# Kernel tuning notes

Hardware: AMD Instinct MI355X
Metric: run time of the kernel (lower is better)

## Reference

```python
import jax, jax.numpy as jnp
import numpy as np

N = 50000      # nodes
E = 400000     # edges (avg degree 8)
C = 128        # dim_single (node_dim)
DP = 64        # dim_pair (edge_dim)
HID = 256      # dim_egnn_hidden
DEPTH = 4      # depth_equivariant
M_IN = 2 * C + DP  # node_mlp / coord_mlp input dim = 320


def setup_inputs() -> dict:
    key = jax.random.key(0)
    ks = jax.random.split(key, 12)
    def w(k, shape, fan):
        return jax.random.normal(k, shape, jnp.float32) / np.float32(np.sqrt(fan))
    return {
        'single': jax.random.normal(ks[0], (N, C), jnp.float32),
        'pair': jax.random.normal(ks[1], (1,), jnp.float32),  # unused (se3t/ipa disabled)
        'coords': jax.random.normal(ks[2], (N, 3), jnp.float32),
        'edge_index': jax.random.randint(ks[3], (2, E), 0, N, jnp.int32),
        'edge_dist': jax.random.uniform(ks[4], (E,), jnp.float32),
        # stacked per-layer EGNN params (leading DEPTH axis, consumed by lax.scan)
        'We1': w(ks[5], (DEPTH, 1, DP), 1), 'be1': jnp.zeros((DEPTH, DP), jnp.float32),
        'We2': w(ks[6], (DEPTH, DP, DP), DP), 'be2': jnp.zeros((DEPTH, DP), jnp.float32),
        'Wn1': w(ks[7], (DEPTH, M_IN, HID), M_IN), 'bn1': jnp.zeros((DEPTH, HID), jnp.float32),
        'Wn2': w(ks[8], (DEPTH, HID, C), HID), 'bn2': jnp.zeros((DEPTH, C), jnp.float32),
        'Wc1': w(ks[9], (DEPTH, M_IN, HID), M_IN), 'bc1': jnp.zeros((DEPTH, HID), jnp.float32),
        'Wc2': w(ks[10], (DEPTH, HID, 1), HID),  # coord_mlp final layer has no bias
        'gamma': jnp.ones((C,), jnp.float32), 'beta': jnp.zeros((C,), jnp.float32),
    }


def _egnn_stack(h, x, edge_index, edge_dist, params):
    src, dst = edge_index[0], edge_index[1]
    n_nodes = h.shape[0]
    def layer(carry, p):
        h, x = carry
        We1, be1, We2, be2, Wn1, bn1, Wn2, bn2, Wc1, bc1, Wc2 = p
        # edge_mlp(edge_dist)
        ea = jax.nn.silu(edge_dist[:, None] @ We1 + be1) @ We2 + be2        # [E, DP]
        # gather -> concat -> MLP (message)
        mi = jnp.concatenate([h[src], h[dst], ea], axis=-1)                 # [E, 2C+DP]
        m = jax.nn.silu(mi @ Wn1 + bn1) @ Wn2 + bn2                         # [E, C]
        h = h + jax.ops.segment_sum(m, dst, num_segments=n_nodes)          # index_add on dst
        # coordinate update
        cw = jax.nn.silu(mi @ Wc1 + bc1) @ Wc2                              # [E, 1]
        x = x + jax.ops.segment_sum(cw * (x[src] - x[dst]), dst, num_segments=n_nodes)
        return (h, x), None
    (h, x), _ = jax.lax.scan(layer, (h, x), params)
    return h, x


def reference(single, pair, coords, edge_index, edge_dist,
              We1, be1, We2, be2, Wn1, bn1, Wn2, bn2, Wc1, bc1, Wc2,
              gamma, beta):
    h, x = _egnn_stack(single, coords, edge_index, edge_dist,
                       (We1, be1, We2, be2, Wn1, bn1, Wn2, bn2, Wc1, bc1, Wc2))
    # final LayerNorm (eps=1e-5, matching nn.LayerNorm default)
    mu = h.mean(-1, keepdims=True)
    var = ((h - mu) ** 2).mean(-1, keepdims=True)
    out = gamma * (h - mu) * jax.lax.rsqrt(var + 1e-5) + beta
    return out, x
```

## Files before the change

kernel.cpp:

```cpp
#include <hip/hip_runtime.h>
#include <hip/hip_bf16.h>
#include <math.h>

#define NN 50000
#define NE 400000
#define CD 128
#define EPB 64
#define HBINS 50176

typedef __attribute__((ext_vector_type(8))) short bf16x8;
typedef __attribute__((ext_vector_type(4))) float f32x4;

__device__ __forceinline__ float silu_f(float z) {
    return z * __builtin_amdgcn_rcpf(1.f + __expf(-z));
}
__device__ __forceinline__ unsigned short f2bf(float x) {
    unsigned int u = __float_as_uint(x);
    u = (u + 0x7FFFu + ((u >> 16) & 1u)) >> 16;
    return (unsigned short)u;
}
__device__ __forceinline__ float bf2f(unsigned short h) {
    return __uint_as_float(((unsigned int)h) << 16);
}
__device__ __forceinline__ unsigned pk_bf16(float a, float b) {
    union { __hip_bfloat162 h2; unsigned u; } cv;
    cv.h2 = __float22bfloat162_rn(make_float2(a, b));
    return cv.u;
}

__global__ __launch_bounds__(256) void hist_kernel(
        const int* __restrict__ dst, int* __restrict__ hist)
{
    int e = blockIdx.x * 256 + threadIdx.x;
    if (e < NE) atomicAdd(&hist[dst[e]], 1);
}

__global__ __launch_bounds__(256) void scan1_kernel(
        const int* __restrict__ hist, int* __restrict__ offs, int* __restrict__ bsum)
{
    __shared__ int sh[256];
    const int t = threadIdx.x;
    const int i = blockIdx.x * 256 + t;
    int v = hist[i];
    sh[t] = v;
    __syncthreads();
    for (int off = 1; off < 256; off <<= 1) {
        int x = (t >= off) ? sh[t - off] : 0;
        __syncthreads();
        sh[t] += x;
        __syncthreads();
    }
    offs[i] = sh[t] - v;
    if (t == 255) bsum[blockIdx.x] = sh[t];
}

__global__ __launch_bounds__(256) void scan2_kernel(int* __restrict__ bsum)
{
    __shared__ int sh[256];
    const int t = threadIdx.x;
    int v = (t < 196) ? bsum[t] : 0;
    sh[t] = v;
    __syncthreads();
    for (int off = 1; off < 256; off <<= 1) {
        int x = (t >= off) ? sh[t - off] : 0;
        __syncthreads();
        sh[t] += x;
        __syncthreads();
    }
    if (t < 196) bsum[t] = sh[t] - v;
}

__global__ __launch_bounds__(256) void scan3_kernel(
        const int* __restrict__ offs, const int* __restrict__ bsum,
        int* __restrict__ cursor)
{
    const int i = blockIdx.x * 256 + threadIdx.x;
    cursor[i] = offs[i] + bsum[blockIdx.x];
}

__global__ __launch_bounds__(256) void scatter_kernel(
        const int* __restrict__ eidx, const float* __restrict__ edist,
        int* __restrict__ cursor,
        int* __restrict__ ssrc, int* __restrict__ sdst, float* __restrict__ sdist)
{
    int e = blockIdx.x * 256 + threadIdx.x;
    if (e < NE) {
        int d = eidx[NE + e];
        int p = atomicAdd(&cursor[d], 1);
        ssrc[p] = eidx[e];
        sdst[p] = d;
        sdist[p] = edist[e];
    }
}

__global__ __launch_bounds__(64) void wbig_prep(
        const float* __restrict__ We2, const float* __restrict__ Wn1,
        const float* __restrict__ Wc1, unsigned short* __restrict__ wbig)
{
    const int l = blockIdx.y;
    const int ntile = blockIdx.x / 10;
    const int ks = blockIdx.x % 10;
    const int lane = threadIdx.x;
    const int n = ntile * 16 + (lane & 15);
    const int kbase = ks * 32 + (lane >> 4) * 8;
    const float* Wn1l = Wn1 + (size_t)l * 320 * 256;
    const float* Wc1l = Wc1 + (size_t)l * 320 * 256;
    const float* We2l = We2 + (size_t)l * 64 * 64;
    const float* W1 = (n < 256) ? Wn1l : Wc1l;
    const int nn = n & 255;
    unsigned short* outp = wbig + ((((size_t)l * 32 + ntile) * 10 + ks) * 64 + lane) * 8;
    #pragma unroll
    for (int j = 0; j < 8; ++j) {
        int k = kbase + j;
        float val;
        if (k < 256) {
            val = W1[(size_t)k * 256 + nn];
        } else {
            int i = k - 256;
            float acc = 0.f;
            #pragma unroll 8
            for (int jj = 0; jj < 64; ++jj)
                acc += We2l[i * 64 + jj] * W1[(size_t)(256 + jj) * 256 + nn];
            val = acc;
        }
        outp[j] = f2bf(val);
    }
}

__global__ __launch_bounds__(64) void wn2_prep(
        const float* __restrict__ Wn2, unsigned short* __restrict__ wn2s)
{
    const int l = blockIdx.y;
    const int ntile = blockIdx.x / 8;
    const int ks = blockIdx.x % 8;
    const int lane = threadIdx.x;
    const int n = ntile * 16 + (lane & 15);
    const int kbase = ks * 32 + (lane >> 4) * 8;
    const float* Wn2l = Wn2 + (size_t)l * 256 * 128;
    unsigned short* outp = wn2s + ((((size_t)l * 8 + ntile) * 8 + ks) * 64 + lane) * 8;
    #pragma unroll
    for (int j = 0; j < 8; ++j)
        outp[j] = f2bf(Wn2l[(size_t)(kbase + j) * 128 + n]);
}

__global__ __launch_bounds__(512) void cep_prep(
        const float* __restrict__ be2,
        const float* __restrict__ Wn1, const float* __restrict__ Wc1,
        const float* __restrict__ bn1, const float* __restrict__ bc1,
        float* __restrict__ cep)
{
    const int l = blockIdx.x;
    const int j = threadIdx.x;
    const int jj = j & 255;
    const float* W1 = ((j < 256) ? Wn1 : Wc1) + (size_t)l * 320 * 256;
    const float* be2l = be2 + l * 64;
    float acc = (j < 256) ? bn1[l * 256 + jj] : bc1[l * 256 + jj];
    #pragma unroll 8
    for (int k = 0; k < 64; ++k)
        acc += be2l[k] * W1[(size_t)(256 + k) * 256 + jj];
    cep[l * 512 + j] = acc;
}

__global__ __launch_bounds__(256) void conv_kernel(
        const float* __restrict__ h, unsigned short* __restrict__ hbf)
{
    const int i = (blockIdx.x * 256 + threadIdx.x) * 4;
    float4 v = *(const float4*)(h + i);
    *(uint2*)(hbf + i) = make_uint2(pk_bf16(v.x, v.y), pk_bf16(v.z, v.w));
}

__global__ __launch_bounds__(512, 4) void edge_kernel(
        const int* __restrict__ ssrc, const int* __restrict__ sdst,
        const float* __restrict__ sdist,
        const float* __restrict__ We1l, const float* __restrict__ be1l,
        const unsigned short* __restrict__ hbf,
        const unsigned short* __restrict__ wbig_l,
        const float* __restrict__ cep_l,
        const float* __restrict__ Wc2l,
        const float* __restrict__ x_in,
        float* __restrict__ Tbar, float* __restrict__ x_out)
{
    __shared__ __align__(16) unsigned short s_A[EPB][328];
    __shared__ __align__(16) unsigned short s_t[EPB][264];
    __shared__ __align__(16) float s_cw[EPB][4];
    __shared__ int s_src[EPB], s_dst[EPB];
    __shared__ unsigned long long s_mask;

    const int tid = threadIdx.x;
    const int eb = blockIdx.x * EPB;

    if (tid < EPB) {
        int dv = sdst[eb + tid];
        s_src[tid] = ssrc[eb + tid];
        s_dst[tid] = dv;
        int nxt = (tid == EPB - 1) ? -1 : sdst[eb + tid + 1];
        unsigned long long mk = __ballot(dv != nxt);
        if (tid == 0) s_mask = mk;
    }
    {
        const int e = tid >> 3;
        const int j0 = (tid & 7) * 8;
        const float d = sdist[eb + e];
        unsigned tmp[4];
        #pragma unroll
        for (int j = 0; j < 4; ++j) {
            float a = silu_f(d * We1l[j0 + 2 * j] + be1l[j0 + 2 * j]);
            float b = silu_f(d * We1l[j0 + 2 * j + 1] + be1l[j0 + 2 * j + 1]);
            tmp[j] = pk_bf16(a, b);
        }
        *(bf16x8*)&s_A[e][j0 + 256] = *(const bf16x8*)tmp;
    }
    __syncthreads();

    #pragma unroll
    for (int it = 0; it < 4; ++it) {
        const int c = tid + it * 512;
        const int row = c >> 5, ch = c & 31;
        const int node = (ch < 16) ? s_src[row] : s_dst[row];
        const int koff = (ch & 15) * 8;
        bf16x8 v = *(const bf16x8*)(hbf + (size_t)node * CD + koff);
        *(bf16x8*)&s_A[row][ch * 8] = v;
    }
    __syncthreads();

    const int wave = tid >> 6, lane = tid & 63;
    const int m = lane & 15, q = lane >> 4;

    f32x4 acc[4][4];
    #pragma unroll
    for (int nt = 0; nt < 4; ++nt)
        #pragma unroll
        for (int mt = 0; mt < 4; ++mt)
            acc[nt][mt] = (f32x4){0.f, 0.f, 0.f, 0.f};

    #pragma unroll
    for (int ks = 0; ks < 10; ++ks) {
        const int koff = ks * 32 + q * 8;
        bf16x8 ef[4];
        #pragma unroll
        for (int mt = 0; mt < 4; ++mt)
            ef[mt] = *(const bf16x8*)&s_A[mt * 16 + m][koff];
        #pragma unroll
        for (int nt = 0; nt < 4; ++nt) {
            bf16x8 wf = *(const bf16x8*)(wbig_l +
                ((size_t)((wave * 4 + nt) * 10 + ks) * 64 + lane) * 8);
            #pragma unroll
            for (int mt = 0; mt < 4; ++mt)
                acc[nt][mt] = __builtin_amdgcn_mfma_f32_16x16x32_bf16(wf, ef[mt], acc[nt][mt], 0, 0, 0);
        }
    }

    if (wave < 4) {
        #pragma unroll
        for (int nt = 0; nt < 4; ++nt) {
            const int c0 = (wave * 4 + nt) * 16 + q * 4;
            const float4 ce = *(const float4*)&cep_l[c0];
            #pragma unroll
            for (int mt = 0; mt < 4; ++mt) {
                float t0 = silu_f(acc[nt][mt][0] + ce.x);
                float t1 = silu_f(acc[nt][mt][1] + ce.y);
                float t2 = silu_f(acc[nt][mt][2] + ce.z);
                float t3 = silu_f(acc[nt][mt][3] + ce.w);
                *(uint2*)&s_t[mt * 16 + m][c0] =
                    make_uint2(pk_bf16(t0, t1), pk_bf16(t2, t3));
            }
        }
    } else {
        float p[4] = {0.f, 0.f, 0.f, 0.f};
        #pragma unroll
        for (int nt = 0; nt < 4; ++nt) {
            const int c0 = (wave * 4 + nt) * 16 + q * 4;
            const float4 ce = *(const float4*)&cep_l[c0];
            const float4 wv = *(const float4*)&Wc2l[c0 - 256];
            #pragma unroll
            for (int mt = 0; mt < 4; ++mt) {
                p[mt] += silu_f(acc[nt][mt][0] + ce.x) * wv.x;
                p[mt] += silu_f(acc[nt][mt][1] + ce.y) * wv.y;
                p[mt] += silu_f(acc[nt][mt][2] + ce.z) * wv.z;
                p[mt] += silu_f(acc[nt][mt][3] + ce.w) * wv.w;
            }
        }
        #pragma unroll
        for (int mt = 0; mt < 4; ++mt) {
            p[mt] += __shfl_xor(p[mt], 16);
            p[mt] += __shfl_xor(p[mt], 32);
        }
        if (lane < 16) {
            #pragma unroll
            for (int mt = 0; mt < 4; ++mt)
                s_cw[mt * 16 + lane][wave - 4] = p[mt];
        }
    }
    __syncthreads();

    if (wave < 2) {
        const unsigned long long mask = s_mask;
        const int colb = wave * 128 + lane * 2;
        float a0 = 0.f, a1 = 0.f;
        #pragma unroll 8
        for (int e = 0; e < EPB; ++e) {
            unsigned v = *(const unsigned*)&s_t[e][colb];
            a0 += bf2f((unsigned short)v);
            a1 += bf2f((unsigned short)(v >> 16));
            if ((mask >> e) & 1ull) {
                int dn = s_dst[e];
                atomicAdd(&Tbar[(size_t)dn * 256 + colb], a0);
                atomicAdd(&Tbar[(size_t)dn * 256 + colb + 1], a1);
                a0 = 0.f; a1 = 0.f;
            }
        }
    } else if (wave == 2) {
        const int e = lane;
        float4 pv = *(const float4*)&s_cw[e][0];
        float cw = pv.x + pv.y + pv.z + pv.w;
        int sn = s_src[e], dn = s_dst[e];
        float dx0 = x_in[sn * 3 + 0] - x_in[dn * 3 + 0];
        float dx1 = x_in[sn * 3 + 1] - x_in[dn * 3 + 1];
        float dx2 = x_in[sn * 3 + 2] - x_in[dn * 3 + 2];
        atomicAdd(&x_out[dn * 3 + 0], cw * dx0);
        atomicAdd(&x_out[dn * 3 + 1], cw * dx1);
        atomicAdd(&x_out[dn * 3 + 2], cw * dx2);
    }
}

__global__ __launch_bounds__(256) void node_kernel(
        const float* __restrict__ Tbar, const int* __restrict__ deg,
        const unsigned short* __restrict__ wn2_l, const float* __restrict__ bn2l,
        float* __restrict__ h, unsigned short* __restrict__ hbf)
{
    const int nb = blockIdx.x * 64;
    const int tid = threadIdx.x;
    const int wave = tid >> 6, lane = tid & 63;
    const int m = lane & 15, q = lane >> 4;

    f32x4 acc[2][4];
    #pragma unroll
    for (int nt = 0; nt < 2; ++nt)
        #pragma unroll
        for (int mt = 0; mt < 4; ++mt)
            acc[nt][mt] = (f32x4){0.f, 0.f, 0.f, 0.f};

    #pragma unroll
    for (int ks = 0; ks < 8; ++ks) {
        bf16x8 af[4];
        #pragma unroll
        for (int mt = 0; mt < 4; ++mt) {
            const int node = nb + mt * 16 + m;
            if (node < NN) {
                const float* tp = Tbar + (size_t)node * 256 + ks * 32 + q * 8;
                float4 f0 = *(const float4*)tp;
                float4 f1 = *(const float4*)(tp + 4);
                unsigned u[4] = { pk_bf16(f0.x, f0.y), pk_bf16(f0.z, f0.w),
                                  pk_bf16(f1.x, f1.y), pk_bf16(f1.z, f1.w) };
                af[mt] = *(const bf16x8*)u;
            } else {
                af[mt] = (bf16x8){0,0,0,0,0,0,0,0};
            }
        }
        #pragma unroll
        for (int nt = 0; nt < 2; ++nt) {
            bf16x8 wf = *(const bf16x8*)(wn2_l +
                ((size_t)((wave * 2 + nt) * 8 + ks) * 64 + lane) * 8);
            #pragma unroll
            for (int mt = 0; mt < 4; ++mt)
                acc[nt][mt] = __builtin_amdgcn_mfma_f32_16x16x32_bf16(af[mt], wf, acc[nt][mt], 0, 0, 0);
        }
    }
    #pragma unroll
    for (int nt = 0; nt < 2; ++nt) {
        const int col = (wave * 2 + nt) * 16 + m;
        const float bb = bn2l[col];
        #pragma unroll
        for (int mt = 0; mt < 4; ++mt) {
            #pragma unroll
            for (int i = 0; i < 4; ++i) {
                const int node = nb + mt * 16 + q * 4 + i;
                if (node < NN) {
                    float val = acc[nt][mt][i] + (float)deg[node] * bb
                              + h[(size_t)node * CD + col];
                    h[(size_t)node * CD + col] = val;
                    hbf[(size_t)node * CD + col] = f2bf(val);
                }
            }
        }
    }
}

__global__ __launch_bounds__(256) void final_kernel(
        const float* __restrict__ h, const float* __restrict__ x,
        const float* __restrict__ gamma, const float* __restrict__ beta,
        float* __restrict__ out)
{
    const int lane = threadIdx.x & 63;
    const int wave = threadIdx.x >> 6;
    const int n = blockIdx.x * 4 + wave;
    float v0 = h[(size_t)n * CD + lane];
    float v1 = h[(size_t)n * CD + 64 + lane];
    float ssum = v0 + v1;
    for (int off = 32; off; off >>= 1) ssum += __shfl_xor(ssum, off);
    float mu = ssum * (1.f / 128.f);
    float d0 = v0 - mu, d1 = v1 - mu;
    float sq = d0 * d0 + d1 * d1;
    for (int off = 32; off; off >>= 1) sq += __shfl_xor(sq, off);
    float rstd = rsqrtf(sq * (1.f / 128.f) + 1e-5f);
    out[(size_t)n * CD + lane]      = gamma[lane]      * d0 * rstd + beta[lane];
    out[(size_t)n * CD + 64 + lane] = gamma[64 + lane] * d1 * rstd + beta[64 + lane];
    if (threadIdx.x < 12) {
        int nn = blockIdx.x * 4 + threadIdx.x / 3;
        int c = threadIdx.x % 3;
        out[(size_t)NN * CD + nn * 3 + c] = x[nn * 3 + c];
    }
}

static inline size_t align_up(size_t v) { return (v + 255) & ~(size_t)255; }

extern "C" void kernel_launch(void* const* d_in, const int* in_sizes, int n_in,
                              void* d_out, int out_size, void* d_ws, size_t ws_size,
                              hipStream_t stream)
{
    const float* single = (const float*)d_in[0];
    const float* coords = (const float*)d_in[2];
    const int*   eidx   = (const int*)d_in[3];
    const float* edist  = (const float*)d_in[4];
    const float* We1 = (const float*)d_in[5];
    const float* be1 = (const float*)d_in[6];
    const float* We2 = (const float*)d_in[7];
    const float* be2 = (const float*)d_in[8];
    const float* Wn1 = (const float*)d_in[9];
    const float* bn1 = (const float*)d_in[10];
    const float* Wn2 = (const float*)d_in[11];
    const float* bn2 = (const float*)d_in[12];
    const float* Wc1 = (const float*)d_in[13];
    const float* bc1 = (const float*)d_in[14];
    const float* Wc2 = (const float*)d_in[15];
    const float* gamma = (const float*)d_in[16];
    const float* beta  = (const float*)d_in[17];
    float* out = (float*)d_out;

    char* w = (char*)d_ws;
    float* h0  = (float*)w;  w += align_up((size_t)NN * CD * 4);
    float* x0  = (float*)w;  w += align_up((size_t)NN * 3 * 4);
    float* x1  = (float*)w;  w += align_up((size_t)NN * 3 * 4);
    unsigned short* hbf  = (unsigned short*)w; w += align_up((size_t)NN * CD * 2);
    unsigned short* wbig = (unsigned short*)w; w += align_up((size_t)4 * 512 * 320 * 2);
    unsigned short* wn2s = (unsigned short*)w; w += align_up((size_t)4 * 256 * 128 * 2);
    float* cep = (float*)w;  w += align_up((size_t)4 * 512 * 4);
    int* hist   = (int*)w;   w += align_up((size_t)HBINS * 4);
    int* offs   = (int*)w;   w += align_up((size_t)HBINS * 4);
    int* cursor = (int*)w;   w += align_up((size_t)HBINS * 4);
    int* bsum   = (int*)w;   w += align_up((size_t)256 * 4);
    int* ssrc   = (int*)w;   w += align_up((size_t)NE * 4);
    int* sdst   = (int*)w;   w += align_up((size_t)NE * 4);
    float* sdist = (float*)w; w += align_up((size_t)NE * 4);
    float* Tbar = (float*)w; w += align_up((size_t)NN * 256 * 4);

    hipMemsetAsync(hist, 0, (size_t)HBINS * 4, stream);
    hist_kernel<<<(NE + 255) / 256, 256, 0, stream>>>(eidx + NE, hist);
    scan1_kernel<<<HBINS / 256, 256, 0, stream>>>(hist, offs, bsum);
    scan2_kernel<<<1, 256, 0, stream>>>(bsum);
    scan3_kernel<<<HBINS / 256, 256, 0, stream>>>(offs, bsum, cursor);
    scatter_kernel<<<(NE + 255) / 256, 256, 0, stream>>>(eidx, edist, cursor, ssrc, sdst, sdist);

    wbig_prep<<<dim3(320, 4), 64, 0, stream>>>(We2, Wn1, Wc1, wbig);
    wn2_prep<<<dim3(64, 4), 64, 0, stream>>>(Wn2, wn2s);
    cep_prep<<<4, 512, 0, stream>>>(be2, Wn1, Wc1, bn1, bc1, cep);

    hipMemcpyAsync(h0, single, (size_t)NN * CD * 4, hipMemcpyDeviceToDevice, stream);
    hipMemcpyAsync(x0, coords, (size_t)NN * 3 * 4, hipMemcpyDeviceToDevice, stream);
    conv_kernel<<<(NN * CD) / 1024, 256, 0, stream>>>(single, hbf);

    float* xc = x0; float* xn = x1;
    for (int l = 0; l < 4; ++l) {
        hipMemsetAsync(Tbar, 0, (size_t)NN * 256 * 4, stream);
        hipMemcpyAsync(xn, xc, (size_t)NN * 3 * 4, hipMemcpyDeviceToDevice, stream);
        edge_kernel<<<NE / EPB, 512, 0, stream>>>(
            ssrc, sdst, sdist,
            We1 + l * 64, be1 + l * 64,
            hbf,
            wbig + (size_t)l * 512 * 320,
            cep + l * 512,
            Wc2 + l * 256,
            xc, Tbar, xn);
        node_kernel<<<(NN + 63) / 64, 256, 0, stream>>>(
            Tbar, hist,
            wn2s + (size_t)l * 256 * 128,
            bn2 + l * CD, h0, hbf);
        float* t = xc; xc = xn; xn = t;
    }
    final_kernel<<<NN / 4, 256, 0, stream>>>(h0, xc, gamma, beta, out);
}
```

Baseline: 1.462 ms.

## Make edge kernel persistent with double-buffered async LDS gathers and MFMA segment reduction

The edge kernel becomes persistent: 512 blocks each loop over a contiguous range of 64-edge tiles. While the current tile is being computed, the next tile's node features are prefetched into double-buffered LDS with global_load_lds, using an XOR swizzle. The per-destination segment sum, previously a serial loop with atomics, is now an MFMA against a 0/1 run-indicator matrix, followed by one atomic per run. This trades occupancy (launch bounds drop to 2 blocks per SM) and adds extra syncs per tile in return for hiding gather latency.

```diff
diff --git a/kernel.cpp b/kernel.cpp
--- a/kernel.cpp
+++ b/kernel.cpp
@@ -5,7 +5,8 @@
 #define NN 50000
 #define NE 400000
 #define CD 128
-#define EPB 64
+#define NT 6250
+#define NB 512
 #define HBINS 50176
 
 typedef __attribute__((ext_vector_type(8))) short bf16x8;
@@ -26,6 +27,11 @@
     union { __hip_bfloat162 h2; unsigned u; } cv;
     cv.h2 = __float22bfloat162_rn(make_float2(a, b));
     return cv.u;
+}
+__device__ __forceinline__ void gload_lds16(const unsigned short* g, unsigned short* l) {
+    __builtin_amdgcn_global_load_lds(
+        (const __attribute__((address_space(1))) unsigned int*)g,
+        (__attribute__((address_space(3))) unsigned int*)l, 16, 0, 0);
 }
 
 __global__ __launch_bounds__(256) void hist_kernel(
@@ -169,7 +175,7 @@
     *(uint2*)(hbf + i) = make_uint2(pk_bf16(v.x, v.y), pk_bf16(v.z, v.w));
 }
 
-__global__ __launch_bounds__(512, 4) void edge_kernel(
+__global__ __launch_bounds__(512, 2) void edge_kernel(
         const int* __restrict__ ssrc, const int* __restrict__ sdst,
         const float* __restrict__ sdist,
         const float* __restrict__ We1l, const float* __restrict__ be1l,
@@ -180,27 +186,37 @@
         const float* __restrict__ x_in,
         float* __restrict__ Tbar, float* __restrict__ x_out)
 {
-    __shared__ __align__(16) unsigned short s_A[EPB][328];
-    __shared__ __align__(16) unsigned short s_t[EPB][264];
-    __shared__ __align__(16) float s_cw[EPB][4];
-    __shared__ int s_src[EPB], s_dst[EPB];
+    __shared__ __align__(16) unsigned short s_h[2][64 * 256];
+    __shared__ __align__(16) unsigned short s_e[2][64][72];
+    __shared__ __align__(16) unsigned short s_tT[256][72];
+    __shared__ __align__(16) unsigned short s_G[64][72];
+    __shared__ __align__(16) float s_cw[64][4];
+    __shared__ int s_sd[2][2][64];
+    __shared__ int s_rdst[64];
     __shared__ unsigned long long s_mask;
 
     const int tid = threadIdx.x;
-    const int eb = blockIdx.x * EPB;
-
-    if (tid < EPB) {
-        int dv = sdst[eb + tid];
-        s_src[tid] = ssrc[eb + tid];
-        s_dst[tid] = dv;
-        int nxt = (tid == EPB - 1) ? -1 : sdst[eb + tid + 1];
-        unsigned long long mk = __ballot(dv != nxt);
-        if (tid == 0) s_mask = mk;
-    }
-    {
-        const int e = tid >> 3;
-        const int j0 = (tid & 7) * 8;
-        const float d = sdist[eb + e];
+    const int wave = tid >> 6, lane = tid & 63;
+    const int m = lane & 15, q = lane >> 4;
+    const int lo = (int)(((long long)blockIdx.x * NT) / NB);
+    const int hi = (int)(((long long)(blockIdx.x + 1) * NT) / NB);
+
+    auto stage_issue = [&](int T) {
+        const int pp = T & 1;
+        #pragma unroll
+        for (int it = 0; it < 4; ++it) {
+            const int slot = it * 512 + wave * 64 + lane;
+            const int row = slot >> 5;
+            const int c = (slot & 31) ^ (row & 7);
+            const int node = s_sd[pp][c >> 4][row];
+            gload_lds16(hbf + (size_t)node * CD + (c & 15) * 8,
+                        &s_h[pp][slot * 8]);
+        }
+    };
+    auto ea_comp = [&](int T) {
+        const int pp = T & 1;
+        const int e = tid >> 3, j0 = (tid & 7) * 8;
+        const float d = sdist[T * 64 + e];
         unsigned tmp[4];
         #pragma unroll
         for (int j = 0; j < 4; ++j) {
@@ -208,118 +224,203 @@
             float b = silu_f(d * We1l[j0 + 2 * j + 1] + be1l[j0 + 2 * j + 1]);
             tmp[j] = pk_bf16(a, b);
         }
-        *(bf16x8*)&s_A[e][j0 + 256] = *(const bf16x8*)tmp;
+        *(bf16x8*)&s_e[pp][e][j0] = *(const bf16x8*)tmp;
+    };
+
+    int sv_c = 0, dv_c = 0, sv_n = 0, dv_n = 0;
+    float xs0 = 0.f, xs1 = 0.f, xs2 = 0.f, xd0 = 0.f, xd1 = 0.f, xd2 = 0.f;
+
+    if (wave == 0) {
+        sv_c = ssrc[lo * 64 + lane];
+        dv_c = sdst[lo * 64 + lane];
+        s_sd[lo & 1][0][lane] = sv_c;
+        s_sd[lo & 1][1][lane] = dv_c;
     }
     __syncthreads();
-
-    #pragma unroll
-    for (int it = 0; it < 4; ++it) {
-        const int c = tid + it * 512;
-        const int row = c >> 5, ch = c & 31;
-        const int node = (ch < 16) ? s_src[row] : s_dst[row];
-        const int koff = (ch & 15) * 8;
-        bf16x8 v = *(const bf16x8*)(hbf + (size_t)node * CD + koff);
-        *(bf16x8*)&s_A[row][ch * 8] = v;
-    }
-    __syncthreads();
-
-    const int wave = tid >> 6, lane = tid & 63;
-    const int m = lane & 15, q = lane >> 4;
-
-    f32x4 acc[4][4];
-    #pragma unroll
-    for (int nt = 0; nt < 4; ++nt)
-        #pragma unroll
-        for (int mt = 0; mt < 4; ++mt)
-            acc[nt][mt] = (f32x4){0.f, 0.f, 0.f, 0.f};
-
-    #pragma unroll
-    for (int ks = 0; ks < 10; ++ks) {
-        const int koff = ks * 32 + q * 8;
-        bf16x8 ef[4];
-        #pragma unroll
-        for (int mt = 0; mt < 4; ++mt)
-            ef[mt] = *(const bf16x8*)&s_A[mt * 16 + m][koff];
-        #pragma unroll
-        for (int nt = 0; nt < 4; ++nt) {
-            bf16x8 wf = *(const bf16x8*)(wbig_l +
-                ((size_t)((wave * 4 + nt) * 10 + ks) * 64 + lane) * 8);
+    stage_issue(lo);
+    ea_comp(lo);
+    if (wave == 0 && lo + 1 < hi) {
+        sv_n = ssrc[(lo + 1) * 64 + lane];
+        dv_n = sdst[(lo + 1) * 64 + lane];
+        s_sd[(lo + 1) & 1][0][lane] = sv_n;
+        s_sd[(lo + 1) & 1][1][lane] = dv_n;
+    }
+
+    for (int T = lo; T < hi; ++T) {
+        const int pb = T & 1;
+
+        for (int i = tid; i < 64 * 72 / 2; i += 512)
+            ((unsigned*)s_G)[i] = 0u;
+        __syncthreads();
+
+        if (wave == 0) {
+            int nxtd = __shfl(dv_c, lane + 1);
+            if (lane == 63) nxtd = -1;
+            unsigned long long mk = __ballot(dv_c != nxtd);
+            int rid = __popcll(mk & ((1ull << lane) - 1ull));
+            s_G[rid][lane ^ ((rid & 3) << 3)] = 0x3F80;
+            if ((mk >> lane) & 1ull) s_rdst[rid] = dv_c;
+            if (lane == 0) s_mask = mk;
+            xs0 = x_in[sv_c * 3];     xs1 = x_in[sv_c * 3 + 1]; xs2 = x_in[sv_c * 3 + 2];
+            xd0 = x_in[dv_c * 3];     xd1 = x_in[dv_c * 3 + 1]; xd2 = x_in[dv_c * 3 + 2];
+        }
+        if (T + 1 < hi) stage_issue(T + 1);
+
+        f32x4 acc[4][4];
+        #pragma unroll
+        for (int nt = 0; nt < 4; ++nt)
             #pragma unroll
             for (int mt = 0; mt < 4; ++mt)
-                acc[nt][mt] = __builtin_amdgcn_mfma_f32_16x16x32_bf16(wf, ef[mt], acc[nt][mt], 0, 0, 0);
-        }
-    }
-
-    if (wave < 4) {
-        #pragma unroll
-        for (int nt = 0; nt < 4; ++nt) {
-            const int c0 = (wave * 4 + nt) * 16 + q * 4;
-            const float4 ce = *(const float4*)&cep_l[c0];
+                acc[nt][mt] = (f32x4){0.f, 0.f, 0.f, 0.f};
+
+        if (wave < 4) {
+            #pragma unroll
+            for (int ks = 0; ks < 10; ++ks) {
+                bf16x8 ef[4];
+                #pragma unroll
+                for (int mt = 0; mt < 4; ++mt) {
+                    const int row = mt * 16 + m;
+                    ef[mt] = (ks < 8)
+                        ? *(const bf16x8*)&s_h[pb][row * 256 + ((ks * 4 + q) ^ (m & 7)) * 8]
+                        : *(const bf16x8*)&s_e[pb][row][(ks - 8) * 32 + q * 8];
+                }
+                #pragma unroll
+                for (int nt = 0; nt < 4; ++nt) {
+                    bf16x8 wf = *(const bf16x8*)(wbig_l +
+                        ((size_t)((wave * 4 + nt) * 10 + ks) * 64 + lane) * 8);
+                    #pragma unroll
+                    for (int mt = 0; mt < 4; ++mt)
+                        acc[nt][mt] = __builtin_amdgcn_mfma_f32_16x16x32_bf16(
+                            ef[mt], wf, acc[nt][mt], 0, 0, 0);
+                }
+            }
+        } else {
+            #pragma unroll
+            for (int ks = 0; ks < 10; ++ks) {
+                bf16x8 ef[4];
+                #pragma unroll
+                for (int mt = 0; mt < 4; ++mt) {
+                    const int row = mt * 16 + m;
+                    ef[mt] = (ks < 8)
+                        ? *(const bf16x8*)&s_h[pb][row * 256 + ((ks * 4 + q) ^ (m & 7)) * 8]
+                        : *(const bf16x8*)&s_e[pb][row][(ks - 8) * 32 + q * 8];
+                }
+                #pragma unroll
+                for (int nt = 0; nt < 4; ++nt) {
+                    bf16x8 wf = *(const bf16x8*)(wbig_l +
+                        ((size_t)((wave * 4 + nt) * 10 + ks) * 64 + lane) * 8);
+                    #pragma unroll
+                    for (int mt = 0; mt < 4; ++mt)
+                        acc[nt][mt] = __builtin_amdgcn_mfma_f32_16x16x32_bf16(
+                            wf, ef[mt], acc[nt][mt], 0, 0, 0);
+                }
+            }
+        }
+        __syncthreads();
+
+        if (wave < 4) {
+            #pragma unroll
+            for (int nt = 0; nt < 4; ++nt) {
+                const int col = (wave * 4 + nt) * 16 + m;
+                const float ce = cep_l[col];
+                #pragma unroll
+                for (int mt = 0; mt < 4; ++mt) {
+                    float t0 = silu_f(acc[nt][mt][0] + ce);
+                    float t1 = silu_f(acc[nt][mt][1] + ce);
+                    float t2 = silu_f(acc[nt][mt][2] + ce);
+                    float t3 = silu_f(acc[nt][mt][3] + ce);
+                    *(uint2*)&s_tT[col][(mt * 16 + q * 4) ^ ((m & 3) << 3)] =
+                        make_uint2(pk_bf16(t0, t1), pk_bf16(t2, t3));
+                }
+            }
+        } else {
+            float pcw[4] = {0.f, 0.f, 0.f, 0.f};
+            #pragma unroll
+            for (int nt = 0; nt < 4; ++nt) {
+                const int c0 = (wave * 4 + nt) * 16 + q * 4;
+                const float4 ce = *(const float4*)&cep_l[c0];
+                const float4 wv = *(const float4*)&Wc2l[c0 - 256];
+                #pragma unroll
+                for (int mt = 0; mt < 4; ++mt) {
+                    pcw[mt] += silu_f(acc[nt][mt][0] + ce.x) * wv.x;
+                    pcw[mt] += silu_f(acc[nt][mt][1] + ce.y) * wv.y;
+                    pcw[mt] += silu_f(acc[nt][mt][2] + ce.z) * wv.z;
+                    pcw[mt] += silu_f(acc[nt][mt][3] + ce.w) * wv.w;
+                }
+            }
             #pragma unroll
             for (int mt = 0; mt < 4; ++mt) {
-                float t0 = silu_f(acc[nt][mt][0] + ce.x);
-                float t1 = silu_f(acc[nt][mt][1] + ce.y);
-                float t2 = silu_f(acc[nt][mt][2] + ce.z);
-                float t3 = silu_f(acc[nt][mt][3] + ce.w);
-                *(uint2*)&s_t[mt * 16 + m][c0] =
-                    make_uint2(pk_bf16(t0, t1), pk_bf16(t2, t3));
-            }
-        }
-    } else {
-        float p[4] = {0.f, 0.f, 0.f, 0.f};
-        #pragma unroll
-        for (int nt = 0; nt < 4; ++nt) {
-            const int c0 = (wave * 4 + nt) * 16 + q * 4;
-            const float4 ce = *(const float4*)&cep_l[c0];
-            const float4 wv = *(const float4*)&Wc2l[c0 - 256];
-            #pragma unroll
-            for (int mt = 0; mt < 4; ++mt) {
-                p[mt] += silu_f(acc[nt][mt][0] + ce.x) * wv.x;
-                p[mt] += silu_f(acc[nt][mt][1] + ce.y) * wv.y;
-                p[mt] += silu_f(acc[nt][mt][2] + ce.z) * wv.z;
-                p[mt] += silu_f(acc[nt][mt][3] + ce.w) * wv.w;
-            }
-        }
-        #pragma unroll
-        for (int mt = 0; mt < 4; ++mt) {
-            p[mt] += __shfl_xor(p[mt], 16);
-            p[mt] += __shfl_xor(p[mt], 32);
-        }
-        if (lane < 16) {
-            #pragma unroll
-            for (int mt = 0; mt < 4; ++mt)
-                s_cw[mt * 16 + lane][wave - 4] = p[mt];
-        }
-    }
-    __syncthreads();
-
-    if (wave < 2) {
-        const unsigned long long mask = s_mask;
-        const int colb = wave * 128 + lane * 2;
-        float a0 = 0.f, a1 = 0.f;
-        #pragma unroll 8
-        for (int e = 0; e < EPB; ++e) {
-            unsigned v = *(const unsigned*)&s_t[e][colb];
-            a0 += bf2f((unsigned short)v);
-            a1 += bf2f((unsigned short)(v >> 16));
-            if ((mask >> e) & 1ull) {
-                int dn = s_dst[e];
-                atomicAdd(&Tbar[(size_t)dn * 256 + colb], a0);
-                atomicAdd(&Tbar[(size_t)dn * 256 + colb + 1], a1);
-                a0 = 0.f; a1 = 0.f;
-            }
-        }
-    } else if (wave == 2) {
-        const int e = lane;
-        float4 pv = *(const float4*)&s_cw[e][0];
-        float cw = pv.x + pv.y + pv.z + pv.w;
-        int sn = s_src[e], dn = s_dst[e];
-        float dx0 = x_in[sn * 3 + 0] - x_in[dn * 3 + 0];
-        float dx1 = x_in[sn * 3 + 1] - x_in[dn * 3 + 1];
-        float dx2 = x_in[sn * 3 + 2] - x_in[dn * 3 + 2];
-        atomicAdd(&x_out[dn * 3 + 0], cw * dx0);
-        atomicAdd(&x_out[dn * 3 + 1], cw * dx1);
-        atomicAdd(&x_out[dn * 3 + 2], cw * dx2);
+                pcw[mt] += __shfl_xor(pcw[mt], 16);
+                pcw[mt] += __shfl_xor(pcw[mt], 32);
+            }
+            if (lane < 16)
+                #pragma unroll
+                for (int mt = 0; mt < 4; ++mt)
+                    s_cw[mt * 16 + lane][wave - 4] = pcw[mt];
+        }
+        __syncthreads();
+
+        {
+            const unsigned long long mask = s_mask;
+            const int nruns = __popcll(mask);
+            f32x4 a2[2][4];
+            #pragma unroll
+            for (int mt2 = 0; mt2 < 2; ++mt2)
+                #pragma unroll
+                for (int nt = 0; nt < 4; ++nt)
+                    a2[mt2][nt] = (f32x4){0.f, 0.f, 0.f, 0.f};
+            #pragma unroll
+            for (int ks = 0; ks < 2; ++ks) {
+                bf16x8 af[2], bfr[4];
+                #pragma unroll
+                for (int mt2 = 0; mt2 < 2; ++mt2)
+                    af[mt2] = *(const bf16x8*)&s_tT[(wave * 2 + mt2) * 16 + m]
+                                               [(ks * 32 + q * 8) ^ ((m & 3) << 3)];
+                #pragma unroll
+                for (int nt = 0; nt < 4; ++nt)
+                    bfr[nt] = *(const bf16x8*)&s_G[nt * 16 + m]
+                                               [(ks * 32 + q * 8) ^ ((m & 3) << 3)];
+                #pragma unroll
+                for (int mt2 = 0; mt2 < 2; ++mt2)
+                    #pragma unroll
+                    for (int nt = 0; nt < 4; ++nt)
+                        a2[mt2][nt] = __builtin_amdgcn_mfma_f32_16x16x32_bf16(
+                            af[mt2], bfr[nt], a2[mt2][nt], 0, 0, 0);
+            }
+            #pragma unroll
+            for (int nt = 0; nt < 4; ++nt) {
+                const int r = nt * 16 + m;
+                if (r < nruns) {
+                    float* bp = Tbar + (size_t)s_rdst[r] * 256;
+                    #pragma unroll
+                    for (int mt2 = 0; mt2 < 2; ++mt2) {
+                        const int c = (wave * 2 + mt2) * 16 + q * 4;
+                        atomicAdd(&bp[c],     a2[mt2][nt][0]);
+                        atomicAdd(&bp[c + 1], a2[mt2][nt][1]);
+                        atomicAdd(&bp[c + 2], a2[mt2][nt][2]);
+                        atomicAdd(&bp[c + 3], a2[mt2][nt][3]);
+                    }
+                }
+            }
+        }
+        if (wave == 0) {
+            const float4 pv = *(const float4*)&s_cw[lane][0];
+            const float cw = pv.x + pv.y + pv.z + pv.w;
+            atomicAdd(&x_out[dv_c * 3],     cw * (xs0 - xd0));
+            atomicAdd(&x_out[dv_c * 3 + 1], cw * (xs1 - xd1));
+            atomicAdd(&x_out[dv_c * 3 + 2], cw * (xs2 - xd2));
+        }
+        if (T + 1 < hi) ea_comp(T + 1);
+        if (wave == 0) {
+            sv_c = sv_n; dv_c = dv_n;
+            if (T + 2 < hi) {
+                sv_n = ssrc[(T + 2) * 64 + lane];
+                dv_n = sdst[(T + 2) * 64 + lane];
+                s_sd[(T + 2) & 1][0][lane] = sv_n;
+                s_sd[(T + 2) & 1][1][lane] = dv_n;
+            }
+        }
+        __syncthreads();
     }
 }
 
@@ -473,7 +574,7 @@
     for (int l = 0; l < 4; ++l) {
         hipMemsetAsync(Tbar, 0, (size_t)NN * 256 * 4, stream);
         hipMemcpyAsync(xn, xc, (size_t)NN * 3 * 4, hipMemcpyDeviceToDevice, stream);
-        edge_kernel<<<NE / EPB, 512, 0, stream>>>(
+        edge_kernel<<<NB, 512, 0, stream>>>(
             ssrc, sdst, sdist,
             We1 + l * 64, be1 + l * 64,
             hbf,
```

Measured after the change: 2.264 ms. +54.9%, slower.

## Segment-reduce edge hidden activations via one-hot MFMA and prefetch weight fragments

Applied to the files above, without the earlier changes.

The serial per-edge loop that summed hidden activations into runs of equal destination and issued atomics from two waves is replaced. Activations are now stored transposed in a swizzled shared buffer and multiplied by a one-hot run-indicator matrix with bf16 MFMA across all eight waves, after which one atomic per run and column is issued. Weight fragments are double-buffered in registers across k-steps, and the MFMA operand order is swapped for waves 0-3 so their outputs come out transposed. This adds shared memory and register pressure and spreads atomics over more waves.

```diff
diff --git a/kernel.cpp b/kernel.cpp
--- a/kernel.cpp
+++ b/kernel.cpp
@@ -181,9 +181,11 @@
         float* __restrict__ Tbar, float* __restrict__ x_out)
 {
     __shared__ __align__(16) unsigned short s_A[EPB][328];
-    __shared__ __align__(16) unsigned short s_t[EPB][264];
+    __shared__ __align__(16) unsigned short s_tT[256][72];
     __shared__ __align__(16) float s_cw[EPB][4];
+    __shared__ __align__(16) unsigned short s_rid[EPB];
     __shared__ int s_src[EPB], s_dst[EPB];
+    __shared__ int s_rdst[EPB];
     __shared__ unsigned long long s_mask;
 
     const int tid = threadIdx.x;
@@ -195,6 +197,9 @@
         s_dst[tid] = dv;
         int nxt = (tid == EPB - 1) ? -1 : sdst[eb + tid + 1];
         unsigned long long mk = __ballot(dv != nxt);
+        int rid = __popcll(mk & ((1ull << tid) - 1ull));
+        s_rid[tid] = (unsigned short)rid;
+        if (dv != nxt) s_rdst[rid] = dv;
         if (tid == 0) s_mask = mk;
     }
     {
@@ -233,35 +238,74 @@
         for (int mt = 0; mt < 4; ++mt)
             acc[nt][mt] = (f32x4){0.f, 0.f, 0.f, 0.f};
 
-    #pragma unroll
-    for (int ks = 0; ks < 10; ++ks) {
-        const int koff = ks * 32 + q * 8;
-        bf16x8 ef[4];
-        #pragma unroll
-        for (int mt = 0; mt < 4; ++mt)
-            ef[mt] = *(const bf16x8*)&s_A[mt * 16 + m][koff];
+    bf16x8 wcur[4], wnxt[4];
+    #pragma unroll
+    for (int nt = 0; nt < 4; ++nt)
+        wcur[nt] = *(const bf16x8*)(wbig_l +
+            ((size_t)((wave * 4 + nt) * 10 + 0) * 64 + lane) * 8);
+
+    if (wave < 4) {
+        #pragma unroll
+        for (int ks = 0; ks < 10; ++ks) {
+            if (ks < 9)
+                #pragma unroll
+                for (int nt = 0; nt < 4; ++nt)
+                    wnxt[nt] = *(const bf16x8*)(wbig_l +
+                        ((size_t)((wave * 4 + nt) * 10 + ks + 1) * 64 + lane) * 8);
+            const int koff = ks * 32 + q * 8;
+            bf16x8 ef[4];
+            #pragma unroll
+            for (int mt = 0; mt < 4; ++mt)
+                ef[mt] = *(const bf16x8*)&s_A[mt * 16 + m][koff];
+            #pragma unroll
+            for (int nt = 0; nt < 4; ++nt)
+                #pragma unroll
+                for (int mt = 0; mt < 4; ++mt)
+                    acc[nt][mt] = __builtin_amdgcn_mfma_f32_16x16x32_bf16(
+                        ef[mt], wcur[nt], acc[nt][mt], 0, 0, 0);
+            if (ks < 9)
+                #pragma unroll
+                for (int nt = 0; nt < 4; ++nt)
+                    wcur[nt] = wnxt[nt];
+        }
+    } else {
+        #pragma unroll
+        for (int ks = 0; ks < 10; ++ks) {
+            if (ks < 9)
+                #pragma unroll
+                for (int nt = 0; nt < 4; ++nt)
+                    wnxt[nt] = *(const bf16x8*)(wbig_l +
+                        ((size_t)((wave * 4 + nt) * 10 + ks + 1) * 64 + lane) * 8);
+            const int koff = ks * 32 + q * 8;
+            bf16x8 ef[4];
+            #pragma unroll
+            for (int mt = 0; mt < 4; ++mt)
+                ef[mt] = *(const bf16x8*)&s_A[mt * 16 + m][koff];
+            #pragma unroll
+            for (int nt = 0; nt < 4; ++nt)
+                #pragma unroll
+                for (int mt = 0; mt < 4; ++mt)
+                    acc[nt][mt] = __builtin_amdgcn_mfma_f32_16x16x32_bf16(
+                        wcur[nt], ef[mt], acc[nt][mt], 0, 0, 0);
+            if (ks < 9)
+                #pragma unroll
+                for (int nt = 0; nt < 4; ++nt)
+                    wcur[nt] = wnxt[nt];
+        }
+    }
+
+    if (wave < 4) {
         #pragma unroll
         for (int nt = 0; nt < 4; ++nt) {
-            bf16x8 wf = *(const bf16x8*)(wbig_l +
-                ((size_t)((wave * 4 + nt) * 10 + ks) * 64 + lane) * 8);
-            #pragma unroll
-            for (int mt = 0; mt < 4; ++mt)
-                acc[nt][mt] = __builtin_amdgcn_mfma_f32_16x16x32_bf16(wf, ef[mt], acc[nt][mt], 0, 0, 0);
-        }
-    }
-
-    if (wave < 4) {
-        #pragma unroll
-        for (int nt = 0; nt < 4; ++nt) {
-            const int c0 = (wave * 4 + nt) * 16 + q * 4;
-            const float4 ce = *(const float4*)&cep_l[c0];
+            const int col = (wave * 4 + nt) * 16 + m;
+            const float ce = cep_l[col];
             #pragma unroll
             for (int mt = 0; mt < 4; ++mt) {
-                float t0 = silu_f(acc[nt][mt][0] + ce.x);
-                float t1 = silu_f(acc[nt][mt][1] + ce.y);
-                float t2 = silu_f(acc[nt][mt][2] + ce.z);
-                float t3 = silu_f(acc[nt][mt][3] + ce.w);
-                *(uint2*)&s_t[mt * 16 + m][c0] =
+                float t0 = silu_f(acc[nt][mt][0] + ce);
+                float t1 = silu_f(acc[nt][mt][1] + ce);
+                float t2 = silu_f(acc[nt][mt][2] + ce);
+                float t3 = silu_f(acc[nt][mt][3] + ce);
+                *(uint2*)&s_tT[col][(mt * 16 + q * 4) ^ ((m & 3) << 3)] =
                     make_uint2(pk_bf16(t0, t1), pk_bf16(t2, t3));
             }
         }
@@ -293,23 +337,60 @@
     }
     __syncthreads();
 
-    if (wave < 2) {
+    {
         const unsigned long long mask = s_mask;
-        const int colb = wave * 128 + lane * 2;
-        float a0 = 0.f, a1 = 0.f;
-        #pragma unroll 8
-        for (int e = 0; e < EPB; ++e) {
-            unsigned v = *(const unsigned*)&s_t[e][colb];
-            a0 += bf2f((unsigned short)v);
-            a1 += bf2f((unsigned short)(v >> 16));
-            if ((mask >> e) & 1ull) {
-                int dn = s_dst[e];
-                atomicAdd(&Tbar[(size_t)dn * 256 + colb], a0);
-                atomicAdd(&Tbar[(size_t)dn * 256 + colb + 1], a1);
-                a0 = 0.f; a1 = 0.f;
+        const int nruns = __popcll(mask);
+        f32x4 a2[2][4];
+        #pragma unroll
+        for (int mt2 = 0; mt2 < 2; ++mt2)
+            #pragma unroll
+            for (int nt = 0; nt < 4; ++nt)
+                a2[mt2][nt] = (f32x4){0.f, 0.f, 0.f, 0.f};
+        #pragma unroll
+        for (int ks = 0; ks < 2; ++ks) {
+            bf16x8 af[2];
+            #pragma unroll
+            for (int mt2 = 0; mt2 < 2; ++mt2)
+                af[mt2] = *(const bf16x8*)&s_tT[(wave * 2 + mt2) * 16 + m]
+                                           [(ks * 32 + q * 8) ^ ((m & 3) << 3)];
+            const unsigned* rp = (const unsigned*)&s_rid[ks * 32 + q * 8];
+            const unsigned r01 = rp[0], r23 = rp[1], r45 = rp[2], r67 = rp[3];
+            #pragma unroll
+            for (int nt = 0; nt < 4; ++nt) {
+                const unsigned n = (unsigned)(nt * 16 + m);
+                unsigned gw[4];
+                gw[0] = ((r01 & 0xFFFFu) == n ? 0x3F80u : 0u) |
+                        ((r01 >> 16)      == n ? 0x3F800000u : 0u);
+                gw[1] = ((r23 & 0xFFFFu) == n ? 0x3F80u : 0u) |
+                        ((r23 >> 16)      == n ? 0x3F800000u : 0u);
+                gw[2] = ((r45 & 0xFFFFu) == n ? 0x3F80u : 0u) |
+                        ((r45 >> 16)      == n ? 0x3F800000u : 0u);
+                gw[3] = ((r67 & 0xFFFFu) == n ? 0x3F80u : 0u) |
+                        ((r67 >> 16)      == n ? 0x3F800000u : 0u);
+                const bf16x8 bfr = *(const bf16x8*)gw;
+                #pragma unroll
+                for (int mt2 = 0; mt2 < 2; ++mt2)
+                    a2[mt2][nt] = __builtin_amdgcn_mfma_f32_16x16x32_bf16(
+                        af[mt2], bfr, a2[mt2][nt], 0, 0, 0);
             }
         }
-    } else if (wave == 2) {
+        #pragma unroll
+        for (int nt = 0; nt < 4; ++nt) {
+            const int r = nt * 16 + m;
+            if (r < nruns) {
+                float* bp = Tbar + (size_t)s_rdst[r] * 256;
+                #pragma unroll
+                for (int mt2 = 0; mt2 < 2; ++mt2) {
+                    const int c = (wave * 2 + mt2) * 16 + q * 4;
+                    atomicAdd(&bp[c],     a2[mt2][nt][0]);
+                    atomicAdd(&bp[c + 1], a2[mt2][nt][1]);
+                    atomicAdd(&bp[c + 2], a2[mt2][nt][2]);
+                    atomicAdd(&bp[c + 3], a2[mt2][nt][3]);
+                }
+            }
+        }
+    }
+    if (wave == 2) {
         const int e = lane;
         float4 pv = *(const float4*)&s_cw[e][0];
         float cw = pv.x + pv.y + pv.z + pv.w;
```

Result: slower. 2.076 ms (+42.0%).
